# Performance work log

Hardware: AMD Instinct MI355X
Metric: run time of the kernel (lower is better)

## Reference

```python
import jax, jax.numpy as jnp
import numpy as np

B, T, D, H, O = 128, 1024, 256, 512, 256

def setup_inputs() -> dict:
    key = jax.random.key(0)
    k0, k1, k2, k3 = jax.random.split(key, 4)
    s_i = 1.0 / np.sqrt(D)
    s_h = 1.0 / np.sqrt(H)
    return {
        "X": jax.random.normal(k0, (B, T, D), jnp.float32),
        "Wi": jax.random.normal(k1, (D, 4 * H), jnp.float32) * s_i,  # input kernel (no bias in flax OptimizedLSTMCell input dense)
        "Wh": jax.random.normal(k2, (H, 4 * H), jnp.float32) * s_h,  # recurrent kernel
        "b": jnp.zeros((4 * H,), jnp.float32),                        # recurrent bias
        "Wd": jax.random.normal(k3, (H, O), jnp.float32) * s_h,      # output Dense kernel
        "bd": jnp.zeros((O,), jnp.float32),                           # output Dense bias
    }

def _lstm_last_hidden(X, Wi, Wh, b):
    # Precompute input projections for all timesteps (same linear map, hoisted out of scan)
    x_proj = jnp.einsum('btd,dg->btg', X, Wi)  # [B, T, 4H]
    h_dim = Wh.shape[0]
    c0 = jnp.zeros((X.shape[0], h_dim), X.dtype)
    h0 = c0

    def step(carry, xt):
        c, h = carry
        y = xt + h @ Wh + b  # [B, 4H]
        i, f, g, o = jnp.split(y, 4, axis=-1)  # flax OptimizedLSTMCell gate order: i, f, g, o
        i = jax.nn.sigmoid(i)
        f = jax.nn.sigmoid(f)
        g = jnp.tanh(g)
        o = jax.nn.sigmoid(o)
        c_new = f * c + i * g
        h_new = o * jnp.tanh(c_new)
        return (c_new, h_new), None

    (c_T, h_T), _ = jax.lax.scan(step, (c0, h0), jnp.swapaxes(x_proj, 0, 1))
    return h_T  # [B, H] = last hidden state

def reference(X, Wi, Wh, b, Wd, bd):
    # Original applies Dense to all timesteps then slices [:, -1, :];
    # Dense is pointwise over time, so applying it to the last hidden is identical math.
    h_last = _lstm_last_hidden(X, Wi, Wh, b)
    return h_last @ Wd + bd  # [B, O]
```

## Files before the change

### kernel.cpp

```cpp
#include <hip/hip_runtime.h>
#include <hip/hip_bf16.h>

#define Bb 128
#define Tt 1024
#define Dd 256
#define Hh 512
#define G4 2048
#define Oo 256

#define NBG 8
#define WPB 16
#define NWG_LAUNCH 256
#define BLOCK 512

#define SPIN_CAP (1u << 16)

typedef __attribute__((ext_vector_type(8))) short short8;
typedef __attribute__((ext_vector_type(4))) float f32x4;
typedef unsigned long long u64;

#define TICK_OFF 0
#define CNT_OFF  2048
#define HBUF_OFF 4096
#define WS_ZERO_BYTES (4096 + Bb*Hh*2)

__device__ __forceinline__ short f2bf(float f) {
  __hip_bfloat16 h = __float2bfloat16(f);
  return *reinterpret_cast<short*>(&h);
}
__device__ __forceinline__ float sigm(float x) {
  return __builtin_amdgcn_rcpf(1.f + __expf(-x));
}
__device__ __forceinline__ float tanh_(float x) {
  return fmaf(2.f, __builtin_amdgcn_rcpf(1.f + __expf(-2.f * x)), -1.f);
}

#define MFMA16(A, B, C) __builtin_amdgcn_mfma_f32_16x16x32_bf16((A), (B), (C), 0, 0, 0)

__global__ __launch_bounds__(BLOCK, 2) void lstm_seq(
    const float* __restrict__ X, const float* __restrict__ Wi,
    const float* __restrict__ Wh, const float* __restrict__ bias,
    char* hbuf, int* cnts, int* tickets)
{
  __shared__ char sH[16 * 1024];
  __shared__ char sX[16 * 512];
  __shared__ unsigned short hstage[16][40];
  __shared__ int sSlot;

  const int tid  = threadIdx.x;
  const int w    = tid >> 6;
  const int lane = tid & 63;

  int myxcc;
  asm volatile("s_getreg_b32 %0, hwreg(HW_REG_XCC_ID)" : "=s"(myxcc));
  myxcc &= 7;
  if (tid == 0) {
    sSlot = __hip_atomic_fetch_add(&tickets[myxcc * 16], 1,
                                   __ATOMIC_RELAXED, __HIP_MEMORY_SCOPE_AGENT);
  }
  __syncthreads();
  const int gjw = sSlot;
  if (gjw >= WPB) return;
  const int bg = myxcc;
  int* cnt = cnts + bg * 32;

  const int cjj  = lane & 15;
  const int kgrp = lane >> 4;
  const int gate = cjj >> 2;
  const int c4   = cjj & 3;
  const int colg = gate * Hh + gjw * 32 + w * 4 + c4;

  short8 wf[24];
#pragma unroll
  for (int kk = 0; kk < 24; ++kk) {
    short8 f;
#pragma unroll
    for (int i = 0; i < 8; ++i) {
      int k = kk * 32 + kgrp * 8 + i;
      float v = (k < Hh) ? Wh[(size_t)k * G4 + colg]
                         : Wi[(size_t)(k - Hh) * G4 + colg];
      f[i] = f2bf(v);
    }
    wf[kk] = f;
  }
  const float bvv = bias[colg];

  const int arow = cjj;
  const int aswz = (arow & 7) << 4;
  float cpr[4] = {0.f, 0.f, 0.f, 0.f};

  const int xrow = tid >> 5, xseg = tid & 31;
  const float* xbase = X + (size_t)(bg * 16 + xrow) * Tt * Dd + xseg * 8;
  f32x4 xA0 = *reinterpret_cast<const f32x4*>(xbase);
  f32x4 xA1 = *reinterpret_cast<const f32x4*>(xbase + 4);
  f32x4 xB0 = *reinterpret_cast<const f32x4*>(xbase + Dd);
  f32x4 xB1 = *reinterpret_cast<const f32x4*>(xbase + Dd + 4);

  auto STEP = [&](int s, f32x4& xv0, f32x4& xv1) {
    const char* hread  = hbuf + (size_t)((s - 1) & 1) * (Bb * Hh * 2);
    char*       hwrite = hbuf + (size_t)(s & 1) * (Bb * Hh * 2);

    {
      short8 xb;
      xb[0] = f2bf(xv0[0]); xb[1] = f2bf(xv0[1]); xb[2] = f2bf(xv0[2]); xb[3] = f2bf(xv0[3]);
      xb[4] = f2bf(xv1[0]); xb[5] = f2bf(xv1[1]); xb[6] = f2bf(xv1[2]); xb[7] = f2bf(xv1[3]);
      *reinterpret_cast<short8*>(sX + xrow * 512 + ((xseg * 16) ^ ((xrow & 7) << 4))) = xb;
    }

    if (s > 1 && tid == 0) {
      const int tgt = WPB * (s - 1);
      unsigned spin = 0;
      while ((int)(__hip_atomic_fetch_add((unsigned*)cnt, 0x10000u,
                                          __ATOMIC_RELAXED,
                                          __HIP_MEMORY_SCOPE_WORKGROUP) & 0xFFFFu) < tgt
             && ++spin < SPIN_CAP) {
        __builtin_amdgcn_s_sleep(2);
      }
    }
    __syncthreads();

    asm volatile("buffer_inv sc0" ::: "memory");
#pragma unroll
    for (int q = 0; q < 2; ++q) {
      int c = tid + q * 512, row = c >> 6, off = c & 63;
      f32x4 v = *reinterpret_cast<const f32x4*>(
          hread + (size_t)(bg * 16 + row) * 1024 + off * 16);
      *reinterpret_cast<f32x4*>(sH + row * 1024 + ((off * 16) ^ ((row & 7) << 4))) = v;
    }
    __syncthreads();

    f32x4 acc_a, acc_b;
#pragma unroll
    for (int m = 0; m < 4; ++m) { acc_a[m] = bvv; acc_b[m] = 0.f; }
#pragma unroll
    for (int kk = 0; kk < 8; ++kk) {
      short8 a = *reinterpret_cast<const short8*>(
          sH + arow * 1024 + ((kk * 64 + kgrp * 16) ^ aswz));
      acc_a = MFMA16(a, wf[kk], acc_a);
    }
#pragma unroll
    for (int kk = 8; kk < 16; ++kk) {
      short8 a = *reinterpret_cast<const short8*>(
          sH + arow * 1024 + ((kk * 64 + kgrp * 16) ^ aswz));
      acc_b = MFMA16(a, wf[kk], acc_b);
    }
#pragma unroll
    for (int kk = 0; kk < 4; ++kk) {
      short8 a = *reinterpret_cast<const short8*>(
          sX + arow * 512 + ((kk * 64 + kgrp * 16) ^ aswz));
      acc_a = MFMA16(a, wf[16 + kk], acc_a);
    }
#pragma unroll
    for (int kk = 4; kk < 8; ++kk) {
      short8 a = *reinterpret_cast<const short8*>(
          sX + arow * 512 + ((kk * 64 + kgrp * 16) ^ aswz));
      acc_b = MFMA16(a, wf[16 + kk], acc_b);
    }
    f32x4 acc;
#pragma unroll
    for (int m = 0; m < 4; ++m) acc[m] = acc_a[m] + acc_b[m];

    float r1[4], r2[4], r3[4];
#pragma unroll
    for (int m = 0; m < 4; ++m) {
      r1[m] = __shfl_xor(acc[m], 4);
      r2[m] = __shfl_xor(acc[m], 8);
      r3[m] = __shfl_xor(r1[m], 8);
    }
    if (cjj < 4) {
#pragma unroll
      for (int m = 0; m < 4; ++m) {
        float ig = sigm(acc[m]), fg = sigm(r1[m]);
        float gg = tanh_(r2[m]), og = sigm(r3[m]);
        float c = fg * cpr[m] + ig * gg;
        cpr[m] = c;
        float hh = og * tanh_(c);
        __hip_bfloat16 hb = __float2bfloat16(hh);
        hstage[kgrp * 4 + m][w * 4 + c4] = *reinterpret_cast<unsigned short*>(&hb);
      }
    }
    __syncthreads();

    if (tid < 64) {
      int row = tid >> 2, chunk = tid & 3;
      f32x4 v = *reinterpret_cast<const f32x4*>(&hstage[row][chunk * 8]);
      *reinterpret_cast<f32x4*>(
          hwrite + ((size_t)(bg * 16 + row) * Hh + gjw * 32 + chunk * 8) * 2) = v;
    }
    __syncthreads();

    if (tid == 0) {
      (void)__hip_atomic_fetch_add(cnt, 1, __ATOMIC_RELAXED,
                                   __HIP_MEMORY_SCOPE_WORKGROUP);
    }

    if (s + 2 <= Tt) {
      xv0 = *reinterpret_cast<const f32x4*>(xbase + (size_t)(s + 1) * Dd);
      xv1 = *reinterpret_cast<const f32x4*>(xbase + (size_t)(s + 1) * Dd + 4);
    }
  };

  for (int s = 1; s <= Tt; s += 2) {
    STEP(s,     xA0, xA1);
    STEP(s + 1, xB0, xB1);
  }
}

__global__ void out_dense(const __hip_bfloat16* __restrict__ hT,
                          const float* __restrict__ Wd,
                          const float* __restrict__ bd,
                          float* __restrict__ out)
{
  __shared__ float hrow[Hh];
  int b = blockIdx.x;
  int o = threadIdx.x;
  for (int k = o; k < Hh; k += Oo)
    hrow[k] = __bfloat162float(hT[(size_t)b * Hh + k]);
  __syncthreads();
  float acc = bd[o];
  for (int k = 0; k < Hh; ++k)
    acc = fmaf(hrow[k], Wd[(size_t)k * Oo + o], acc);
  out[(size_t)b * Oo + o] = acc;
}

extern "C" void kernel_launch(void* const* d_in, const int* in_sizes, int n_in,
                              void* d_out, int out_size, void* d_ws, size_t ws_size,
                              hipStream_t stream) {
  (void)in_sizes; (void)n_in; (void)out_size; (void)ws_size;
  const float* X  = (const float*)d_in[0];
  const float* Wi = (const float*)d_in[1];
  const float* Wh = (const float*)d_in[2];
  const float* b  = (const float*)d_in[3];
  const float* Wd = (const float*)d_in[4];
  const float* bd = (const float*)d_in[5];
  float* out = (float*)d_out;

  char* ws = (char*)d_ws;
  int* tickets = (int*)(ws + TICK_OFF);
  int* cnts    = (int*)(ws + CNT_OFF);
  char* hbuf   = ws + HBUF_OFF;

  hipMemsetAsync(d_ws, 0, WS_ZERO_BYTES, stream);
  lstm_seq<<<NWG_LAUNCH, BLOCK, 0, stream>>>(X, Wi, Wh, b, hbuf, cnts, tickets);
  out_dense<<<Bb, Oo, 0, stream>>>((const __hip_bfloat16*)hbuf, Wd, bd, out);
}
```

Baseline: 2.659 ms.

## Replace shared counter with per-producer flags and overlap input GEMM with wait

Replaces the single per-batch-group atomic counter with one flag per producer workgroup. Each wave now polls only the two producer flags whose h slice it needs, then loads just that slice into shared memory. The input-projection MFMAs are moved ahead of the spin wait so they overlap with waiting on other workgroups. One barrier before signalling is removed by using a vmcnt wait on the writing threads. This trades contention on one atomic for more polling traffic, and the modified barrier structure risks subtle ordering issues across workgroups.

Measured after the change: 3.028 ms. 1.14x slower.

```diff
diff --git a/kernel.cpp b/kernel.cpp
--- a/kernel.cpp
+++ b/kernel.cpp
@@ -13,16 +13,16 @@
 #define NWG_LAUNCH 256
 #define BLOCK 512
 
-#define SPIN_CAP (1u << 16)
+#define SPIN_CAP 65536u
 
 typedef __attribute__((ext_vector_type(8))) short short8;
 typedef __attribute__((ext_vector_type(4))) float f32x4;
 typedef unsigned long long u64;
 
 #define TICK_OFF 0
-#define CNT_OFF  2048
-#define HBUF_OFF 4096
-#define WS_ZERO_BYTES (4096 + Bb*Hh*2)
+#define FLAG_OFF 2048
+#define HBUF_OFF 12288
+#define WS_ZERO_BYTES (12288 + Bb*Hh*2)
 
 __device__ __forceinline__ short f2bf(float f) {
   __hip_bfloat16 h = __float2bfloat16(f);
@@ -40,7 +40,7 @@
 __global__ __launch_bounds__(BLOCK, 2) void lstm_seq(
     const float* __restrict__ X, const float* __restrict__ Wi,
     const float* __restrict__ Wh, const float* __restrict__ bias,
-    char* hbuf, int* cnts, int* tickets)
+    char* hbuf, int* flags, int* tickets)
 {
   __shared__ char sH[16 * 1024];
   __shared__ char sX[16 * 512];
@@ -62,7 +62,8 @@
   const int gjw = sSlot;
   if (gjw >= WPB) return;
   const int bg = myxcc;
-  int* cnt = cnts + bg * 32;
+  int* bgflags = flags + bg * 256;
+  int* myflag  = bgflags + gjw * 16;
 
   const int cjj  = lane & 15;
   const int kgrp = lane >> 4;
@@ -88,6 +89,9 @@
   const int arow = cjj;
   const int aswz = (arow & 7) << 4;
   float cpr[4] = {0.f, 0.f, 0.f, 0.f};
+
+  const int hsrow = lane & 15;
+  const int hsq   = lane >> 4;
 
   const int xrow = tid >> 5, xseg = tid & 31;
   const float* xbase = X + (size_t)(bg * 16 + xrow) * Tt * Dd + xseg * 8;
@@ -106,32 +110,53 @@
       xb[4] = f2bf(xv1[0]); xb[5] = f2bf(xv1[1]); xb[6] = f2bf(xv1[2]); xb[7] = f2bf(xv1[3]);
       *reinterpret_cast<short8*>(sX + xrow * 512 + ((xseg * 16) ^ ((xrow & 7) << 4))) = xb;
     }
-
-    if (s > 1 && tid == 0) {
-      const int tgt = WPB * (s - 1);
+    __syncthreads();
+
+    f32x4 acc_a, acc_b;
+#pragma unroll
+    for (int m = 0; m < 4; ++m) { acc_a[m] = bvv; acc_b[m] = 0.f; }
+#pragma unroll
+    for (int kk = 0; kk < 4; ++kk) {
+      short8 a = *reinterpret_cast<const short8*>(
+          sX + arow * 512 + ((kk * 64 + kgrp * 16) ^ aswz));
+      acc_a = MFMA16(a, wf[16 + kk], acc_a);
+    }
+#pragma unroll
+    for (int kk = 4; kk < 8; ++kk) {
+      short8 a = *reinterpret_cast<const short8*>(
+          sX + arow * 512 + ((kk * 64 + kgrp * 16) ^ aswz));
+      acc_b = MFMA16(a, wf[16 + kk], acc_b);
+    }
+
+    if (s > 1) {
+      const unsigned tgt = (unsigned)(s - 1);
       unsigned spin = 0;
-      while ((int)(__hip_atomic_fetch_add((unsigned*)cnt, 0x10000u,
-                                          __ATOMIC_RELAXED,
-                                          __HIP_MEMORY_SCOPE_WORKGROUP) & 0xFFFFu) < tgt
-             && ++spin < SPIN_CAP) {
-        __builtin_amdgcn_s_sleep(2);
+      bool done = (lane >= 2);
+      unsigned* fp = (unsigned*)(bgflags + (w * 2 + (lane & 1)) * 16);
+      while (!__all(done)) {
+        if (!done) {
+          unsigned v = __hip_atomic_fetch_add(fp, 0x10000u, __ATOMIC_RELAXED,
+                                              __HIP_MEMORY_SCOPE_WORKGROUP);
+          done = ((v & 0xFFFFu) >= tgt);
+        }
+        if (!__all(done)) {
+          if (++spin >= SPIN_CAP) break;
+          __builtin_amdgcn_s_sleep(1);
+        }
       }
     }
+
+    asm volatile("buffer_inv sc0" ::: "memory");
+#pragma unroll
+    for (int p = 0; p < 2; ++p) {
+      int q = hsq + 4 * p;
+      f32x4 v = *reinterpret_cast<const f32x4*>(
+          hread + (size_t)(bg * 16 + hsrow) * 1024 + w * 128 + q * 16);
+      *reinterpret_cast<f32x4*>(
+          sH + hsrow * 1024 + ((w * 128 + q * 16) ^ ((hsrow & 7) << 4))) = v;
+    }
     __syncthreads();
 
-    asm volatile("buffer_inv sc0" ::: "memory");
-#pragma unroll
-    for (int q = 0; q < 2; ++q) {
-      int c = tid + q * 512, row = c >> 6, off = c & 63;
-      f32x4 v = *reinterpret_cast<const f32x4*>(
-          hread + (size_t)(bg * 16 + row) * 1024 + off * 16);
-      *reinterpret_cast<f32x4*>(sH + row * 1024 + ((off * 16) ^ ((row & 7) << 4))) = v;
-    }
-    __syncthreads();
-
-    f32x4 acc_a, acc_b;
-#pragma unroll
-    for (int m = 0; m < 4; ++m) { acc_a[m] = bvv; acc_b[m] = 0.f; }
 #pragma unroll
     for (int kk = 0; kk < 8; ++kk) {
       short8 a = *reinterpret_cast<const short8*>(
@@ -143,18 +168,6 @@
       short8 a = *reinterpret_cast<const short8*>(
           sH + arow * 1024 + ((kk * 64 + kgrp * 16) ^ aswz));
       acc_b = MFMA16(a, wf[kk], acc_b);
-    }
-#pragma unroll
-    for (int kk = 0; kk < 4; ++kk) {
-      short8 a = *reinterpret_cast<const short8*>(
-          sX + arow * 512 + ((kk * 64 + kgrp * 16) ^ aswz));
-      acc_a = MFMA16(a, wf[16 + kk], acc_a);
-    }
-#pragma unroll
-    for (int kk = 4; kk < 8; ++kk) {
-      short8 a = *reinterpret_cast<const short8*>(
-          sX + arow * 512 + ((kk * 64 + kgrp * 16) ^ aswz));
-      acc_b = MFMA16(a, wf[16 + kk], acc_b);
     }
     f32x4 acc;
 #pragma unroll
@@ -186,12 +199,11 @@
       f32x4 v = *reinterpret_cast<const f32x4*>(&hstage[row][chunk * 8]);
       *reinterpret_cast<f32x4*>(
           hwrite + ((size_t)(bg * 16 + row) * Hh + gjw * 32 + chunk * 8) * 2) = v;
-    }
-    __syncthreads();
-
-    if (tid == 0) {
-      (void)__hip_atomic_fetch_add(cnt, 1, __ATOMIC_RELAXED,
-                                   __HIP_MEMORY_SCOPE_WORKGROUP);
+      asm volatile("s_waitcnt vmcnt(0)" ::: "memory");
+      if (tid == 0) {
+        (void)__hip_atomic_fetch_add(myflag, 1, __ATOMIC_RELAXED,
+                                     __HIP_MEMORY_SCOPE_WORKGROUP);
+      }
     }
 
     if (s + 2 <= Tt) {
@@ -237,10 +249,10 @@
 
   char* ws = (char*)d_ws;
   int* tickets = (int*)(ws + TICK_OFF);
-  int* cnts    = (int*)(ws + CNT_OFF);
+  int* flags   = (int*)(ws + FLAG_OFF);
   char* hbuf   = ws + HBUF_OFF;
 
   hipMemsetAsync(d_ws, 0, WS_ZERO_BYTES, stream);
-  lstm_seq<<<NWG_LAUNCH, BLOCK, 0, stream>>>(X, Wi, Wh, b, hbuf, cnts, tickets);
+  lstm_seq<<<NWG_LAUNCH, BLOCK, 0, stream>>>(X, Wi, Wh, b, hbuf, flags, tickets);
   out_dense<<<Bb, Oo, 0, stream>>>((const __hip_bfloat16*)hbuf, Wd, bd, out);
 }
```
